# Kernel tuning notes

Hardware: AMD Instinct MI355X
Metric: run time of the kernel (lower is better)

## Reference

```python
import jax, jax.numpy as jnp
import numpy as np

B, T, C, H = 4, 2048, 2048, 16
DH = C // H  # 128

def setup_inputs() -> dict:
    key = jax.random.key(0)
    ks = jax.random.split(key, 5)
    s_in = 1.0 / np.sqrt(C)
    return {
        "x": jax.random.normal(ks[0], (B, T, C), dtype=jnp.float32),
        "qkv_w": jax.random.uniform(ks[1], (3 * C, C), jnp.float32, -s_in, s_in),
        "qkv_b": jax.random.uniform(ks[2], (3 * C,), jnp.float32, -s_in, s_in),
        "proj_w": jax.random.uniform(ks[3], (C, C), jnp.float32, -s_in, s_in),
        "proj_b": jax.random.uniform(ks[4], (C,), jnp.float32, -s_in, s_in),
    }

def reference(x, qkv_w, qkv_b, proj_w, proj_b):
    b, t, _ = x.shape
    qkv = x @ qkv_w.T + qkv_b                     # [B,T,3C]
    q, k, v = jnp.split(qkv, 3, axis=-1)
    # [B,T,C] -> [B,H,T,Dh]
    q = q.reshape(b, t, H, DH).transpose(0, 2, 1, 3)
    k = k.reshape(b, t, H, DH).transpose(0, 2, 1, 3)
    v = v.reshape(b, t, H, DH).transpose(0, 2, 1, 3)
    scores = jnp.einsum('bhqd,bhkd->bhqk', q, k) / jnp.sqrt(jnp.float32(DH))
    causal = jnp.tril(jnp.ones((t, t), dtype=bool))  # [T,T]
    scores = jnp.where(causal[None, None], scores, jnp.finfo(scores.dtype).min)
    att = jax.nn.softmax(scores, axis=-1)
    out = jnp.einsum('bhqk,bhkd->bhqd', att, v)   # [B,H,T,Dh]
    out = out.transpose(0, 2, 1, 3).reshape(b, t, C)
    return out @ proj_w.T + proj_b
```

## Files before the change

### kernel.cpp

```cpp
#include <hip/hip_runtime.h>
#include <stdint.h>


typedef __attribute__((ext_vector_type(8))) short bf8_t;
typedef __attribute__((ext_vector_type(4))) float f4_t;

__device__ __forceinline__ short f2bf(float f) {
  union { float f; uint32_t u; } x; x.f = f;
  uint32_t r = x.u + 0x7fffu + ((x.u >> 16) & 1u);
  return (short)(r >> 16);
}

#define GLD16(gp, lp) __builtin_amdgcn_global_load_lds( \
    (const __attribute__((address_space(1))) void*)(gp), \
    (__attribute__((address_space(3))) void*)(lp), 16, 0, 0)

#define QSCALE (0.08838834764831845f * 1.4426950408889634f)

__global__ __launch_bounds__(256) void cast_f32_bf16(
    const float* __restrict__ in, short* __restrict__ out, int n4) {
  int i = blockIdx.x * blockDim.x + threadIdx.x;
  if (i < n4) {
    float4 v = ((const float4*)in)[i];
    short4 o;
    o.x = f2bf(v.x); o.y = f2bf(v.y); o.z = f2bf(v.z); o.w = f2bf(v.w);
    ((short4*)out)[i] = o;
  }
}

template <int MODE>
__global__ __launch_bounds__(256) void gemm_bt(
    const short* __restrict__ A, const short* __restrict__ Bw,
    const float* __restrict__ bias, float* __restrict__ Cout,
    short* __restrict__ Qo, short* __restrict__ Ko, short* __restrict__ Vo,
    int M, int N, int K) {
  __shared__ __attribute__((aligned(16))) short lA[8192];
  __shared__ __attribute__((aligned(16))) short lB[8192];
  const int tid = threadIdx.x;
  const int lane = tid & 63, wave = tid >> 6;
  const int quad = lane >> 4, l16 = lane & 15;
  const int wm = wave >> 1, wn = wave & 1;
  const int m0 = blockIdx.y * 128, n0 = blockIdx.x * 128;
  const int which = (MODE == 0) ? (n0 >> 11) : -1;
  const bool swapAB = (MODE == 0) && (which == 2);

  const f4_t fz = {0.f, 0.f, 0.f, 0.f};
  f4_t acc[4][4];
#pragma unroll
  for (int i = 0; i < 4; ++i)
#pragma unroll
    for (int j = 0; j < 4; ++j) acc[i][j] = fz;

  for (int k0 = 0; k0 < K; k0 += 64) {
    __syncthreads();
#pragma unroll
    for (int r = 0; r < 4; ++r) {
      const int off = tid * 16 + r * 4096;
      const int kk = off >> 13;
      const int row = (off >> 6) & 127;
      const int col = kk * 32 + ((off & 63) >> 1);
      GLD16(A + (size_t)(m0 + row) * K + (k0 + col), (char*)lA + off);
      GLD16(Bw + (size_t)(n0 + row) * K + (k0 + col), (char*)lB + off);
    }
    __syncthreads();
#pragma unroll
    for (int kk = 0; kk < 2; ++kk) {
      bf8_t af[4], bfr[4];
#pragma unroll
      for (int i = 0; i < 4; ++i) {
        af[i]  = *(const bf8_t*)(lA + kk * 4096 + (wm * 64 + i * 16 + l16) * 32 + quad * 8);
        bfr[i] = *(const bf8_t*)(lB + kk * 4096 + (wn * 64 + i * 16 + l16) * 32 + quad * 8);
      }
      if (!swapAB) {
#pragma unroll
        for (int i = 0; i < 4; ++i)
#pragma unroll
          for (int j = 0; j < 4; ++j)
            acc[i][j] = __builtin_amdgcn_mfma_f32_16x16x32_bf16(af[i], bfr[j], acc[i][j], 0, 0, 0);
      } else {
#pragma unroll
        for (int i = 0; i < 4; ++i)
#pragma unroll
          for (int j = 0; j < 4; ++j)
            acc[i][j] = __builtin_amdgcn_mfma_f32_16x16x32_bf16(bfr[i], af[j], acc[i][j], 0, 0, 0);
      }
    }
  }

  if (MODE == 1) {
    const int mb = m0 + wm * 64, nb = n0 + wn * 64;
#pragma unroll
    for (int i = 0; i < 4; ++i) {
#pragma unroll
      for (int r = 0; r < 4; ++r) {
        const int m = mb + i * 16 + quad * 4 + r;
#pragma unroll
        for (int j = 0; j < 4; ++j) {
          const int n = nb + j * 16 + l16;
          Cout[(size_t)m * N + n] = acc[i][j][r] + bias[n];
        }
      }
    }
  } else if (!swapAB) {
    const int mb = m0 + wm * 64, nb = n0 + wn * 64;
    const int b = m0 >> 11;
    const int h = (n0 & 2047) >> 7;
    short* dst = (which == 0) ? Qo : Ko;
    const float sc = (which == 0) ? QSCALE : 1.0f;
#pragma unroll
    for (int i = 0; i < 4; ++i) {
#pragma unroll
      for (int r = 0; r < 4; ++r) {
        const int t = (mb + i * 16 + quad * 4 + r) & 2047;
#pragma unroll
        for (int j = 0; j < 4; ++j) {
          const int n = nb + j * 16 + l16;
          const int d = n & 127;
          dst[((size_t)((b * 16 + h) * 2048 + t)) * 128 + d] =
              f2bf((acc[i][j][r] + bias[n]) * sc);
        }
      }
    }
  } else {
    const int b = m0 >> 11;
    const int h = (n0 & 2047) >> 7;
#pragma unroll
    for (int i = 0; i < 4; ++i) {
#pragma unroll
      for (int r = 0; r < 4; ++r) {
        const int doff = wn * 64 + i * 16 + quad * 4 + r;
        const int n = n0 + doff;
        const float bb = bias[n];
#pragma unroll
        for (int j = 0; j < 4; ++j) {
          const int t = (m0 & 2047) + wm * 64 + j * 16 + l16;
          Vo[((size_t)((b * 16 + h) * 128 + doff)) * 2048 + t] =
              f2bf(acc[i][j][r] + bb);
        }
      }
    }
  }
}

__global__ __launch_bounds__(256) void attn_fwd(
    const short* __restrict__ Qg, const short* __restrict__ Kg,
    const short* __restrict__ Vtg, short* __restrict__ Og) {
  __shared__ __attribute__((aligned(16))) short lK[64 * 128];
  __shared__ __attribute__((aligned(16))) short lV[128 * 64];
  __shared__ __attribute__((aligned(16))) short lP[4 * 2048];
  const int tid = threadIdx.x;
  const int lane = tid & 63, wave = tid >> 6;
  const int quad = lane >> 4, l16 = lane & 15;
  const int p = blockIdx.x & 7, bh = blockIdx.x >> 3;
  const size_t baseK = (size_t)bh * (2048 * 128);
  const size_t baseV = (size_t)bh * (128 * 2048);
  const int x7 = l16 & 7;
  const int b = bh >> 4, h = bh & 15;
  short* lPw = lP + wave * 2048;
  const f4_t fz = {0.f, 0.f, 0.f, 0.f};

  for (int job = 0; job < 2; ++job) {
    const int bx = job ? (15 - p) : p;
    const int q0 = bx * 128;
    const int qw = q0 + wave * 32;

    bf8_t qf[2][4];
#pragma unroll
    for (int m = 0; m < 2; ++m)
#pragma unroll
      for (int dc = 0; dc < 4; ++dc)
        qf[m][dc] = *(const bf8_t*)(Qg + baseK + (size_t)(qw + m * 16 + l16) * 128 + dc * 32 + quad * 8);

    f4_t o[2][8];
#pragma unroll
    for (int m = 0; m < 2; ++m)
#pragma unroll
      for (int n = 0; n < 8; ++n) o[m][n] = fz;
    float lsum[2][4];
#pragma unroll
    for (int m = 0; m < 2; ++m)
#pragma unroll
      for (int r = 0; r < 4; ++r) lsum[m][r] = 0.f;

    const int ktmax = 2 * bx + 1;
    for (int kt = 0; kt <= ktmax; ++kt) {
      const int k0 = kt * 64;
      __syncthreads();
#pragma unroll
      for (int r = 0; r < 4; ++r) {
        const int off = tid * 16 + r * 4096;
        const int rowK = off >> 8;
        const int lcK = ((off >> 4) & 15) ^ (rowK & 7);
        GLD16(Kg + baseK + (size_t)(k0 + rowK) * 128 + lcK * 8, (char*)lK + off);
        const int dV = off >> 7;
        const int lcV = ((off >> 4) & 7) ^ (dV & 7);
        GLD16(Vtg + baseV + (size_t)dV * 2048 + (k0 + lcV * 8), (char*)lV + off);
      }
      __syncthreads();
      if (k0 >= qw + 32) continue;

      f4_t s[2][4];
#pragma unroll
      for (int m = 0; m < 2; ++m)
#pragma unroll
        for (int g = 0; g < 4; ++g) s[m][g] = fz;
#pragma unroll
      for (int g = 0; g < 4; ++g)
#pragma unroll
        for (int dc = 0; dc < 4; ++dc) {
          bf8_t kf = *(const bf8_t*)(lK + (g * 16 + l16) * 128 + (((dc * 4 + quad) ^ x7) << 3));
          s[0][g] = __builtin_amdgcn_mfma_f32_16x16x32_bf16(qf[0][dc], kf, s[0][g], 0, 0, 0);
          s[1][g] = __builtin_amdgcn_mfma_f32_16x16x32_bf16(qf[1][dc], kf, s[1][g], 0, 0, 0);
        }
#pragma unroll
      for (int m = 0; m < 2; ++m) {
        const int qbase = qw + m * 16;
        const bool nomask = (k0 + 63 <= qbase);
#pragma unroll
        for (int g = 0; g < 4; ++g) {
          const int key = k0 + g * 16 + l16;
#pragma unroll
          for (int r = 0; r < 4; ++r) {
            float pv = exp2f(s[m][g][r]);
            if (!nomask && key > qbase + quad * 4 + r) pv = 0.f;
            lsum[m][r] += pv;
            const int row = quad * 4 + r;
            lPw[m * 1024 + row * 64 + (((g * 2 + (l16 >> 3)) ^ (row & 7)) << 3) + x7] = f2bf(pv);
          }
        }
      }
      bf8_t pa[2][2];
#pragma unroll
      for (int m = 0; m < 2; ++m)
#pragma unroll
        for (int kc = 0; kc < 2; ++kc)
          pa[m][kc] = *(const bf8_t*)(lPw + m * 1024 + l16 * 64 + (((kc * 4 + quad) ^ x7) << 3));
#pragma unroll
      for (int n = 0; n < 8; ++n)
#pragma unroll
        for (int kc = 0; kc < 2; ++kc) {
          bf8_t vf = *(const bf8_t*)(lV + (n * 16 + l16) * 64 + (((kc * 4 + quad) ^ x7) << 3));
          o[0][n] = __builtin_amdgcn_mfma_f32_16x16x32_bf16(pa[0][kc], vf, o[0][n], 0, 0, 0);
          o[1][n] = __builtin_amdgcn_mfma_f32_16x16x32_bf16(pa[1][kc], vf, o[1][n], 0, 0, 0);
        }
    }
#pragma unroll
    for (int m = 0; m < 2; ++m)
#pragma unroll
      for (int r = 0; r < 4; ++r) {
        float v = lsum[m][r];
        v += __shfl_xor(v, 1, 64);
        v += __shfl_xor(v, 2, 64);
        v += __shfl_xor(v, 4, 64);
        v += __shfl_xor(v, 8, 64);
        const float inv = 1.f / v;
        const int t = qw + m * 16 + quad * 4 + r;
        const size_t orow = ((size_t)(b * 2048 + t)) * 2048 + h * 128;
#pragma unroll
        for (int n = 0; n < 8; ++n)
          Og[orow + n * 16 + l16] = f2bf(o[m][n][r] * inv);
      }
  }
}

extern "C" void kernel_launch(void* const* d_in, const int* in_sizes, int n_in,
                              void* d_out, int out_size, void* d_ws, size_t ws_size,
                              hipStream_t stream) {
  const float* x      = (const float*)d_in[0];
  const float* qkv_w  = (const float*)d_in[1];
  const float* qkv_b  = (const float*)d_in[2];
  const float* proj_w = (const float*)d_in[3];
  const float* proj_b = (const float*)d_in[4];
  float* out = (float*)d_out;

  char* ws = (char*)d_ws;
  short* xb    = (short*)(ws);
  short* wqkv  = (short*)(ws + 33554432);
  short* wproj = (short*)(ws + 58720256);
  short* qb    = (short*)(ws + 67108864);
  short* kb    = (short*)(ws + 100663296);
  short* vb    = (short*)(ws + 134217728);
  short* attb  = (short*)(ws + 167772160);

  cast_f32_bf16<<<16384, 256, 0, stream>>>(x, xb, 16777216 / 4);
  cast_f32_bf16<<<12288, 256, 0, stream>>>(qkv_w, wqkv, 12582912 / 4);
  cast_f32_bf16<<<4096, 256, 0, stream>>>(proj_w, wproj, 4194304 / 4);

  gemm_bt<0><<<dim3(48, 64), 256, 0, stream>>>(xb, wqkv, qkv_b, nullptr,
                                               qb, kb, vb, 8192, 6144, 2048);
  attn_fwd<<<512, 256, 0, stream>>>(qb, kb, vb, attb);
  gemm_bt<1><<<dim3(16, 64), 256, 0, stream>>>(attb, wproj, proj_b, out,
                                               nullptr, nullptr, nullptr, 8192, 2048, 2048);
}
```

Baseline: 663.0 us.

## Merge cast kernels, init accumulators with bias, precompute load offsets

Replaces the three separate fp32-to-bf16 cast launches with a single kernel covering all three tensors, removing launch gaps. The GEMM now seeds its accumulators with the bias instead of adding it in the epilogue. Both the GEMM and attention kernels precompute per-thread global load offsets once and advance base pointers each iteration, cutting address arithmetic in the inner loops. These changes mostly trim overhead; the cast kernel gains a per-thread branch to pick its source tensor.

```diff
diff --git a/kernel.cpp b/kernel.cpp
--- a/kernel.cpp
+++ b/kernel.cpp
@@ -17,15 +17,21 @@
 
 #define QSCALE (0.08838834764831845f * 1.4426950408889634f)
 
-__global__ __launch_bounds__(256) void cast_f32_bf16(
-    const float* __restrict__ in, short* __restrict__ out, int n4) {
+__global__ __launch_bounds__(256) void cast3_f32_bf16(
+    const float* __restrict__ a, const float* __restrict__ b,
+    const float* __restrict__ c, short* __restrict__ oa,
+    short* __restrict__ ob, short* __restrict__ oc,
+    int na4, int nb4, int nc4) {
   int i = blockIdx.x * blockDim.x + threadIdx.x;
-  if (i < n4) {
-    float4 v = ((const float4*)in)[i];
-    short4 o;
-    o.x = f2bf(v.x); o.y = f2bf(v.y); o.z = f2bf(v.z); o.w = f2bf(v.w);
-    ((short4*)out)[i] = o;
-  }
+  const float* src; short* dst; int idx;
+  if (i < na4) { src = a; dst = oa; idx = i; }
+  else if (i < na4 + nb4) { src = b; dst = ob; idx = i - na4; }
+  else if (i < na4 + nb4 + nc4) { src = c; dst = oc; idx = i - na4 - nb4; }
+  else return;
+  float4 v = ((const float4*)src)[idx];
+  short4 o;
+  o.x = f2bf(v.x); o.y = f2bf(v.y); o.z = f2bf(v.z); o.w = f2bf(v.w);
+  ((short4*)dst)[idx] = o;
 }
 
 template <int MODE>
@@ -44,24 +50,48 @@
   const int which = (MODE == 0) ? (n0 >> 11) : -1;
   const bool swapAB = (MODE == 0) && (which == 2);
 
-  const f4_t fz = {0.f, 0.f, 0.f, 0.f};
   f4_t acc[4][4];
-#pragma unroll
-  for (int i = 0; i < 4; ++i)
-#pragma unroll
-    for (int j = 0; j < 4; ++j) acc[i][j] = fz;
+  if (!swapAB) {
+#pragma unroll
+    for (int j = 0; j < 4; ++j) {
+      const float b0 = bias[n0 + wn * 64 + j * 16 + l16];
+      const f4_t bv = {b0, b0, b0, b0};
+#pragma unroll
+      for (int i = 0; i < 4; ++i) acc[i][j] = bv;
+    }
+  } else {
+#pragma unroll
+    for (int i = 0; i < 4; ++i)
+#pragma unroll
+      for (int r = 0; r < 4; ++r) {
+        const float b0 = bias[n0 + wn * 64 + i * 16 + quad * 4 + r];
+#pragma unroll
+        for (int j = 0; j < 4; ++j) acc[i][j][r] = b0;
+      }
+  }
+
+  const char* baseA = (const char*)(A + (size_t)m0 * K);
+  const char* baseB = (const char*)(Bw + (size_t)n0 * K);
+  uint32_t voff[4];
+#pragma unroll
+  for (int r = 0; r < 4; ++r) {
+    const int off = tid * 16 + r * 4096;
+    const int kk = off >> 13;
+    const int row = (off >> 6) & 127;
+    const int col = kk * 32 + ((off & 63) >> 1);
+    voff[r] = (uint32_t)(row * K + col) * 2u;
+  }
 
   for (int k0 = 0; k0 < K; k0 += 64) {
     __syncthreads();
 #pragma unroll
     for (int r = 0; r < 4; ++r) {
       const int off = tid * 16 + r * 4096;
-      const int kk = off >> 13;
-      const int row = (off >> 6) & 127;
-      const int col = kk * 32 + ((off & 63) >> 1);
-      GLD16(A + (size_t)(m0 + row) * K + (k0 + col), (char*)lA + off);
-      GLD16(Bw + (size_t)(n0 + row) * K + (k0 + col), (char*)lB + off);
-    }
+      GLD16(baseA + voff[r], (char*)lA + off);
+      GLD16(baseB + voff[r], (char*)lB + off);
+    }
+    baseA += 128;
+    baseB += 128;
     __syncthreads();
 #pragma unroll
     for (int kk = 0; kk < 2; ++kk) {
@@ -97,7 +127,7 @@
 #pragma unroll
         for (int j = 0; j < 4; ++j) {
           const int n = nb + j * 16 + l16;
-          Cout[(size_t)m * N + n] = acc[i][j][r] + bias[n];
+          Cout[(size_t)m * N + n] = acc[i][j][r];
         }
       }
     }
@@ -114,10 +144,9 @@
         const int t = (mb + i * 16 + quad * 4 + r) & 2047;
 #pragma unroll
         for (int j = 0; j < 4; ++j) {
-          const int n = nb + j * 16 + l16;
-          const int d = n & 127;
+          const int d = (nb + j * 16 + l16) & 127;
           dst[((size_t)((b * 16 + h) * 2048 + t)) * 128 + d] =
-              f2bf((acc[i][j][r] + bias[n]) * sc);
+              f2bf(acc[i][j][r] * sc);
         }
       }
     }
@@ -129,13 +158,11 @@
 #pragma unroll
       for (int r = 0; r < 4; ++r) {
         const int doff = wn * 64 + i * 16 + quad * 4 + r;
-        const int n = n0 + doff;
-        const float bb = bias[n];
 #pragma unroll
         for (int j = 0; j < 4; ++j) {
           const int t = (m0 & 2047) + wm * 64 + j * 16 + l16;
           Vo[((size_t)((b * 16 + h) * 128 + doff)) * 2048 + t] =
-              f2bf(acc[i][j][r] + bb);
+              f2bf(acc[i][j][r]);
         }
       }
     }
@@ -159,6 +186,18 @@
   short* lPw = lP + wave * 2048;
   const f4_t fz = {0.f, 0.f, 0.f, 0.f};
 
+  uint32_t vK[4], vV[4];
+#pragma unroll
+  for (int r = 0; r < 4; ++r) {
+    const int off = tid * 16 + r * 4096;
+    const int rowK = off >> 8;
+    const int lcK = ((off >> 4) & 15) ^ (rowK & 7);
+    vK[r] = (uint32_t)(rowK * 128 + lcK * 8) * 2u;
+    const int dV = off >> 7;
+    const int lcV = ((off >> 4) & 7) ^ (dV & 7);
+    vV[r] = (uint32_t)(dV * 2048 + lcV * 8) * 2u;
+  }
+
   for (int job = 0; job < 2; ++job) {
     const int bx = job ? (15 - p) : p;
     const int q0 = bx * 128;
@@ -182,6 +221,8 @@
 #pragma unroll
       for (int r = 0; r < 4; ++r) lsum[m][r] = 0.f;
 
+    const char* kbase = (const char*)(Kg + baseK);
+    const char* vbase = (const char*)(Vtg + baseV);
     const int ktmax = 2 * bx + 1;
     for (int kt = 0; kt <= ktmax; ++kt) {
       const int k0 = kt * 64;
@@ -189,13 +230,11 @@
 #pragma unroll
       for (int r = 0; r < 4; ++r) {
         const int off = tid * 16 + r * 4096;
-        const int rowK = off >> 8;
-        const int lcK = ((off >> 4) & 15) ^ (rowK & 7);
-        GLD16(Kg + baseK + (size_t)(k0 + rowK) * 128 + lcK * 8, (char*)lK + off);
-        const int dV = off >> 7;
-        const int lcV = ((off >> 4) & 7) ^ (dV & 7);
-        GLD16(Vtg + baseV + (size_t)dV * 2048 + (k0 + lcV * 8), (char*)lV + off);
-      }
+        GLD16(kbase + vK[r], (char*)lK + off);
+        GLD16(vbase + vV[r], (char*)lV + off);
+      }
+      kbase += 16384;
+      vbase += 128;
       __syncthreads();
       if (k0 >= qw + 32) continue;
 
@@ -282,9 +321,8 @@
   short* vb    = (short*)(ws + 134217728);
   short* attb  = (short*)(ws + 167772160);
 
-  cast_f32_bf16<<<16384, 256, 0, stream>>>(x, xb, 16777216 / 4);
-  cast_f32_bf16<<<12288, 256, 0, stream>>>(qkv_w, wqkv, 12582912 / 4);
-  cast_f32_bf16<<<4096, 256, 0, stream>>>(proj_w, wproj, 4194304 / 4);
+  cast3_f32_bf16<<<32768, 256, 0, stream>>>(x, qkv_w, proj_w, xb, wqkv, wproj,
+                                            4194304, 3145728, 1048576);
 
   gemm_bt<0><<<dim3(48, 64), 256, 0, stream>>>(xb, wqkv, qkv_b, nullptr,
                                                qb, kb, vb, 8192, 6144, 2048);
```

New measurement: 603.9 us. 1.1x faster.
